# Performance work log

Measured on AMD Instinct MI355X. Metric: run time of the kernel, lower is better.

## Reference

```python
import jax, jax.numpy as jnp
import numpy as np

H = 8
DQ = 32
DK = 32
DV = 32
DC = DQ + DK  # concat dim for additive attention


def setup_inputs() -> dict:
    key = jax.random.key(0)
    ks = jax.random.split(key, 8)
    bs, Lq, Lk = 2, 384, 384
    q = jax.random.normal(ks[0], (bs, Lq, H * DQ), jnp.float32)
    k = jax.random.normal(ks[1], (bs, Lk, H * DK), jnp.float32)
    v = jax.random.normal(ks[2], (bs, Lk, H * DV), jnp.float32)
    q_sequence_lengths = jax.random.randint(ks[3], (bs,), 1, Lq + 1, dtype=jnp.int32)
    k_sequence_lengths = jax.random.randint(ks[4], (bs,), 1, Lk + 1, dtype=jnp.int32)
    bound = 1.0 / np.sqrt(DC)
    w1 = jax.random.uniform(ks[5], (H, DC, DC), jnp.float32, -bound, bound)
    b1 = jax.random.uniform(ks[6], (H, DC), jnp.float32, -bound, bound)
    w2 = jax.random.uniform(ks[7], (H, DC), jnp.float32, -1.0, 1.0)
    return {"q": q, "k": k, "v": v,
            "q_sequence_lengths": q_sequence_lengths,
            "k_sequence_lengths": k_sequence_lengths,
            "w1": w1, "b1": b1, "w2": w2}


def reference(q, k, v, q_sequence_lengths, k_sequence_lengths, w1, b1, w2):
    bs, Lq, _ = q.shape
    Lk = k.shape[1]
    # split heads: (b, h, L, d)
    qh = q.reshape(bs, Lq, H, DQ).transpose(0, 2, 1, 3)
    kh = k.reshape(bs, Lk, H, DK).transpose(0, 2, 1, 3)
    vh = v.reshape(bs, Lk, H, DV).transpose(0, 2, 1, 3)
    # additive scores: tanh(cat(q_i, k_j) @ W1 + b1) @ w2
    # cat @ W1 == q @ W1[:DQ] + k @ W1[DQ:]  (avoids materializing the cat)
    qW = jnp.einsum('bhqd,hde->bhqe', qh, w1[:, :DQ, :])
    kW = jnp.einsum('bhkd,hde->bhke', kh, w1[:, DQ:, :])
    hid = jnp.tanh(qW[:, :, :, None, :] + kW[:, :, None, :, :] + b1[None, :, None, None, :])  # (b,h,q,k,DC)
    scores = jnp.einsum('bhqke,he->bhqk', hid, w2)
    # key-side length mask (end padded)
    kmask = jnp.arange(Lk)[None, :] < k_sequence_lengths[:, None]  # (b, Lk)
    scores = jnp.where(kmask[:, None, None, :], scores, jnp.float32(-1e9))
    att = jax.nn.softmax(scores, axis=-1)  # (b,h,q,k)
    out = jnp.einsum('bhqk,bhkd->bqhd', att, vh)  # (b,q,h,DV)
    # query-side length mask zeros out padded query rows
    qmask = jnp.arange(Lq)[None, :] < q_sequence_lengths[:, None]  # (b, Lq)
    out = out * qmask[:, :, None, None].astype(out.dtype)
    return out.reshape(bs, Lq, H * DV), att
```

## Files before the change

kernel.cpp:

```cpp
#include <hip/hip_runtime.h>

#define NH 8
#define LQ 384
#define LK 384
#define BS 2
#define NQE (BS*NH*LQ*64)

__global__ __launch_bounds__(256) void precompute_kernel(
    const float* __restrict__ qin, const float* __restrict__ kin,
    const float* __restrict__ w1, const float* __restrict__ b1,
    float* __restrict__ ws)
{
    __shared__ float tile[64][65];
    if (blockIdx.x < 1536) {
        int gid = blockIdx.x * 256 + threadIdx.x;
        int e  = gid & 63;
        int qe = gid >> 6;
        int qq = qe % LQ;
        int bh = qe / LQ;
        int b = bh >> 3, h = bh & 7;
        const float* qrow = qin + ((size_t)(b * LQ + qq)) * (NH * 32) + h * 32;
        const float* w1c  = w1 + (size_t)(h * 64) * 64 + e;
        float acc = 0.f;
        #pragma unroll
        for (int d = 0; d < 32; ++d)
            acc = __builtin_fmaf(qrow[d], w1c[d * 64], acc);
        ws[gid] = __expf(acc + acc);
    } else {
        int bid = blockIdx.x - 1536;
        int bh = bid / 6, kt = bid % 6;
        int b = bh >> 3, h = bh & 7;
        int k0 = kt * 64;
        int lane = threadIdx.x & 63, w = threadIdx.x >> 6;
        float w1c[32];
        const float* w1p = w1 + (size_t)(h * 64 + 32) * 64 + lane;
        #pragma unroll
        for (int d = 0; d < 32; ++d) w1c[d] = w1p[d * 64];
        float bv = b1[h * 64 + lane];
        for (int s = 0; s < 16; ++s) {
            int krel = w * 16 + s;
            const float* krow = kin + ((size_t)(b * LK + k0 + krel)) * (NH * 32) + h * 32;
            float acc = bv;
            #pragma unroll
            for (int d = 0; d < 32; ++d)
                acc = __builtin_fmaf(krow[d], w1c[d], acc);
            tile[krel][lane] = __expf(acc + acc);
        }
        __syncthreads();
        float* wk = ws + NQE + (size_t)bh * 64 * LK + k0;
        for (int s = 0; s < 16; ++s) {
            int e = w * 16 + s;
            wk[(size_t)e * LK + lane] = tile[lane][e];
        }
    }
}

__global__ __launch_bounds__(256, 4) void attn_kernel(
    const float* __restrict__ vin,
    const int* __restrict__ qlens, const int* __restrict__ klens,
    const float* __restrict__ w2g, const float* __restrict__ ws,
    float* __restrict__ outg, float* __restrict__ attg)
{
    __shared__ __align__(16) float ek[16 * LK];
    __shared__ __align__(16) float att_s[8][LK];
    __shared__ __align__(16) float eqs[8 * 64];
    __shared__ __align__(16) float w2s[64];

    const int tid = threadIdx.x, wave = tid >> 6, lane = tid & 63;
    const int bh = blockIdx.x / 48, tile = blockIdx.x % 48;
    const int b = bh >> 3, h = bh & 7;
    const int q0 = tile * 8;
    const int klen = klens[b], qlen = qlens[b];

    if (tid < 128) ((float4*)eqs)[tid] = ((const float4*)(ws + ((size_t)bh * LQ + q0) * 64))[tid];
    else if (tid < 144) ((float4*)w2s)[tid - 128] = ((const float4*)(w2g + h * 64))[tid - 128];

    float sc[2][6];
    #pragma unroll
    for (int i = 0; i < 2; ++i)
        #pragma unroll
        for (int j = 0; j < 6; ++j) sc[i][j] = 0.f;

    const float* ekg = ws + NQE + (size_t)bh * 64 * LK;
    for (int ec = 0; ec < 4; ++ec) {
        __syncthreads();
        const float4* src = (const float4*)(ekg + (size_t)ec * 16 * LK);
        #pragma unroll
        for (int r = 0; r < 6; ++r)
            ((float4*)ek)[tid + r * 256] = src[tid + r * 256];
        __syncthreads();
        #pragma unroll 2
        for (int e = 0; e < 16; ++e) {
            float kv[6];
            #pragma unroll
            for (int j = 0; j < 6; ++j) kv[j] = ek[e * LK + j * 64 + lane];
            float wv = w2s[ec * 16 + e];
            #pragma unroll
            for (int i = 0; i < 2; ++i) {
                float qv = eqs[(wave * 2 + i) * 64 + ec * 16 + e];
                #pragma unroll
                for (int j = 0; j < 6; ++j) {
                    float E = qv * kv[j];
                    float r = __builtin_amdgcn_rcpf(1.0f + E);
                    sc[i][j] = __builtin_fmaf(wv, r, sc[i][j]);
                }
            }
        }
    }

    #pragma unroll
    for (int i = 0; i < 2; ++i) {
        int row = wave * 2 + i, q = q0 + row;
        float s_[6], p[6];
        float m = -3.4e38f;
        #pragma unroll
        for (int j = 0; j < 6; ++j) {
            int kk = j * 64 + lane;
            float v = -2.0f * sc[i][j];
            s_[j] = (kk < klen) ? v : -3.4e38f;
            m = fmaxf(m, s_[j]);
        }
        #pragma unroll
        for (int off = 32; off >= 1; off >>= 1) m = fmaxf(m, __shfl_xor(m, off));
        float ssum = 0.f;
        #pragma unroll
        for (int j = 0; j < 6; ++j) {
            int kk = j * 64 + lane;
            p[j] = (kk < klen) ? __expf(s_[j] - m) : 0.f;
            ssum += p[j];
        }
        #pragma unroll
        for (int off = 32; off >= 1; off >>= 1) ssum += __shfl_xor(ssum, off);
        float inv = __builtin_amdgcn_rcpf(ssum);
        float* arow = att_s[row];
        float* ag = attg + ((size_t)(bh * LQ + q)) * LK;
        #pragma unroll
        for (int j = 0; j < 6; ++j) {
            float a = p[j] * inv;
            arow[j * 64 + lane] = a;
            ag[j * 64 + lane]   = a;
        }
    }

    const int dv = lane & 31, halfk = lane >> 5;
    float oacc[2] = {0.f, 0.f};
    for (int c = 0; c < 2; ++c) {
        __syncthreads();
        const float4* vg = (const float4*)(vin + ((size_t)(b * LK + c * 192)) * (NH * 32) + h * 32);
        #pragma unroll
        for (int r = 0; r < 6; ++r) {
            int fidx = tid + r * 256;
            int kk = fidx >> 3, d4 = fidx & 7;
            ((float4*)ek)[fidx] = vg[(size_t)kk * 64 + d4];
        }
        __syncthreads();
        #pragma unroll
        for (int i = 0; i < 2; ++i) {
            const float* ar = att_s[wave * 2 + i] + c * 192 + halfk * 96;
            const float* vb = ek + (halfk * 96) * 32 + dv;
            float acc = 0.f;
            #pragma unroll
            for (int kk = 0; kk < 96; kk += 4) {
                float4 a4 = *(const float4*)(ar + kk);
                acc = __builtin_fmaf(a4.x, vb[(kk + 0) * 32], acc);
                acc = __builtin_fmaf(a4.y, vb[(kk + 1) * 32], acc);
                acc = __builtin_fmaf(a4.z, vb[(kk + 2) * 32], acc);
                acc = __builtin_fmaf(a4.w, vb[(kk + 3) * 32], acc);
            }
            oacc[i] += acc;
        }
    }
    #pragma unroll
    for (int i = 0; i < 2; ++i) oacc[i] += __shfl_xor(oacc[i], 32);
    if (lane < 32) {
        #pragma unroll
        for (int i = 0; i < 2; ++i) {
            int q = q0 + wave * 2 + i;
            outg[((size_t)(b * LQ + q)) * (NH * 32) + h * 32 + dv] = (q < qlen) ? oacc[i] : 0.f;
        }
    }
}

extern "C" void kernel_launch(void* const* d_in, const int* in_sizes, int n_in,
                              void* d_out, int out_size, void* d_ws, size_t ws_size,
                              hipStream_t stream) {
    const float* q    = (const float*)d_in[0];
    const float* k    = (const float*)d_in[1];
    const float* v    = (const float*)d_in[2];
    const int*   qlen = (const int*)d_in[3];
    const int*   klen = (const int*)d_in[4];
    const float* w1   = (const float*)d_in[5];
    const float* b1   = (const float*)d_in[6];
    const float* w2   = (const float*)d_in[7];
    float* out = (float*)d_out;
    float* att = out + (size_t)BS * LQ * NH * 32;
    float* ws  = (float*)d_ws;

    precompute_kernel<<<1632, 256, 0, stream>>>(q, k, w1, b1, ws);
    attn_kernel<<<768, 256, 0, stream>>>(v, qlen, klen, w2, ws, out, att);
}
```

Baseline: 113.5 us.

## Merge four reciprocals per score step, fuse q projection into attention kernel

The score loop now combines four terms w_i/(1+E_i) into one fraction, so it needs a single reciprocal per four hidden units instead of one each, cutting transcendental-unit pressure. The q-side exp projection moves out of the precompute kernel and into the attention kernel, which removes a workspace round trip and shrinks the precompute grid to the k side only. The P·V loop is re-laid out so each lane reads float4 of V and writes float4 outputs, with a shuffle reduction across k groups. The risk is overflow or precision loss in the product of four (1+E) terms when the exponentials get large.

```diff
diff --git a/kernel.cpp b/kernel.cpp
--- a/kernel.cpp
+++ b/kernel.cpp
@@ -4,61 +4,48 @@
 #define LQ 384
 #define LK 384
 #define BS 2
-#define NQE (BS*NH*LQ*64)
-
-__global__ __launch_bounds__(256) void precompute_kernel(
-    const float* __restrict__ qin, const float* __restrict__ kin,
-    const float* __restrict__ w1, const float* __restrict__ b1,
-    float* __restrict__ ws)
+
+__global__ __launch_bounds__(256) void pre_ek_kernel(
+    const float* __restrict__ kin, const float* __restrict__ w1,
+    const float* __restrict__ b1, float* __restrict__ ws)
 {
-    __shared__ float tile[64][65];
-    if (blockIdx.x < 1536) {
-        int gid = blockIdx.x * 256 + threadIdx.x;
-        int e  = gid & 63;
-        int qe = gid >> 6;
-        int qq = qe % LQ;
-        int bh = qe / LQ;
-        int b = bh >> 3, h = bh & 7;
-        const float* qrow = qin + ((size_t)(b * LQ + qq)) * (NH * 32) + h * 32;
-        const float* w1c  = w1 + (size_t)(h * 64) * 64 + e;
-        float acc = 0.f;
-        #pragma unroll
-        for (int d = 0; d < 32; ++d)
-            acc = __builtin_fmaf(qrow[d], w1c[d * 64], acc);
-        ws[gid] = __expf(acc + acc);
-    } else {
-        int bid = blockIdx.x - 1536;
-        int bh = bid / 6, kt = bid % 6;
-        int b = bh >> 3, h = bh & 7;
-        int k0 = kt * 64;
-        int lane = threadIdx.x & 63, w = threadIdx.x >> 6;
-        float w1c[32];
-        const float* w1p = w1 + (size_t)(h * 64 + 32) * 64 + lane;
-        #pragma unroll
-        for (int d = 0; d < 32; ++d) w1c[d] = w1p[d * 64];
-        float bv = b1[h * 64 + lane];
-        for (int s = 0; s < 16; ++s) {
-            int krel = w * 16 + s;
-            const float* krow = kin + ((size_t)(b * LK + k0 + krel)) * (NH * 32) + h * 32;
-            float acc = bv;
-            #pragma unroll
-            for (int d = 0; d < 32; ++d)
-                acc = __builtin_fmaf(krow[d], w1c[d], acc);
-            tile[krel][lane] = __expf(acc + acc);
-        }
-        __syncthreads();
-        float* wk = ws + NQE + (size_t)bh * 64 * LK + k0;
-        for (int s = 0; s < 16; ++s) {
-            int e = w * 16 + s;
-            wk[(size_t)e * LK + lane] = tile[lane][e];
-        }
+    __shared__ float tile[32][65];
+    const int bid = blockIdx.x;
+    const int bh = bid / 12, kt = bid % 12;
+    const int b = bh >> 3, h = bh & 7;
+    const int k0 = kt * 32;
+    const int lane = threadIdx.x & 63, w = threadIdx.x >> 6;
+
+    float w1c[32];
+    const float* w1p = w1 + (size_t)(h * 64 + 32) * 64 + lane;
+    #pragma unroll
+    for (int d = 0; d < 32; ++d) w1c[d] = w1p[d * 64];
+    const float bv = b1[h * 64 + lane];
+
+    #pragma unroll
+    for (int s = 0; s < 8; ++s) {
+        int kr = w * 8 + s;
+        const float* krow = kin + ((size_t)(b * LK + k0 + kr)) * (NH * 32) + h * 32;
+        float acc = bv;
+        #pragma unroll
+        for (int d = 0; d < 32; ++d) acc = __builtin_fmaf(krow[d], w1c[d], acc);
+        tile[kr][lane] = __expf(acc + acc);
+    }
+    __syncthreads();
+    float* wk = ws + (size_t)bh * 64 * LK + k0;
+    const int k32 = lane & 31, eh = lane >> 5;
+    #pragma unroll
+    for (int s2 = 0; s2 < 8; ++s2) {
+        int e = w * 16 + s2 * 2 + eh;
+        wk[(size_t)e * LK + k32] = tile[k32][e];
     }
 }
 
 __global__ __launch_bounds__(256, 4) void attn_kernel(
-    const float* __restrict__ vin,
+    const float* __restrict__ qin, const float* __restrict__ vin,
     const int* __restrict__ qlens, const int* __restrict__ klens,
-    const float* __restrict__ w2g, const float* __restrict__ ws,
+    const float* __restrict__ w1, const float* __restrict__ w2g,
+    const float* __restrict__ ws,
     float* __restrict__ outg, float* __restrict__ attg)
 {
     __shared__ __align__(16) float ek[16 * LK];
@@ -72,8 +59,24 @@
     const int q0 = tile * 8;
     const int klen = klens[b], qlen = qlens[b];
 
-    if (tid < 128) ((float4*)eqs)[tid] = ((const float4*)(ws + ((size_t)bh * LQ + q0) * 64))[tid];
-    else if (tid < 144) ((float4*)w2s)[tid - 128] = ((const float4*)(w2g + h * 64))[tid - 128];
+    if (tid < 16) ((float4*)w2s)[tid] = ((const float4*)(w2g + h * 64))[tid];
+
+    {
+        float w1c[32];
+        const float* w1q = w1 + (size_t)(h * 64) * 64 + lane;
+        #pragma unroll
+        for (int d = 0; d < 32; ++d) w1c[d] = w1q[d * 64];
+        const float* qr0 = qin + ((size_t)(b * LQ + q0 + wave)) * (NH * 32) + h * 32;
+        const float* qr1 = qr0 + 4 * (NH * 32);
+        float a0 = 0.f, a1 = 0.f;
+        #pragma unroll
+        for (int d = 0; d < 32; ++d) {
+            a0 = __builtin_fmaf(qr0[d], w1c[d], a0);
+            a1 = __builtin_fmaf(qr1[d], w1c[d], a1);
+        }
+        eqs[wave * 64 + lane]       = __expf(a0 + a0);
+        eqs[(wave + 4) * 64 + lane] = __expf(a1 + a1);
+    }
 
     float sc[2][6];
     #pragma unroll
@@ -81,7 +84,10 @@
         #pragma unroll
         for (int j = 0; j < 6; ++j) sc[i][j] = 0.f;
 
-    const float* ekg = ws + NQE + (size_t)bh * 64 * LK;
+    const float* ekg = ws + (size_t)bh * 64 * LK;
+    const float4* eq0p = (const float4*)(eqs + (wave * 2 + 0) * 64);
+    const float4* eq1p = (const float4*)(eqs + (wave * 2 + 1) * 64);
+
     for (int ec = 0; ec < 4; ++ec) {
         __syncthreads();
         const float4* src = (const float4*)(ekg + (size_t)ec * 16 * LK);
@@ -89,20 +95,39 @@
         for (int r = 0; r < 6; ++r)
             ((float4*)ek)[tid + r * 256] = src[tid + r * 256];
         __syncthreads();
-        #pragma unroll 2
-        for (int e = 0; e < 16; ++e) {
-            float kv[6];
+        #pragma unroll
+        for (int q4 = 0; q4 < 4; ++q4) {
+            float4 wv  = ((const float4*)w2s)[ec * 4 + q4];
+            float4 eqv0 = eq0p[ec * 4 + q4];
+            float4 eqv1 = eq1p[ec * 4 + q4];
+            const float* ekb = ek + (q4 * 4) * LK + lane;
             #pragma unroll
-            for (int j = 0; j < 6; ++j) kv[j] = ek[e * LK + j * 64 + lane];
-            float wv = w2s[ec * 16 + e];
-            #pragma unroll
-            for (int i = 0; i < 2; ++i) {
-                float qv = eqs[(wave * 2 + i) * 64 + ec * 16 + e];
-                #pragma unroll
-                for (int j = 0; j < 6; ++j) {
-                    float E = qv * kv[j];
-                    float r = __builtin_amdgcn_rcpf(1.0f + E);
-                    sc[i][j] = __builtin_fmaf(wv, r, sc[i][j]);
+            for (int j = 0; j < 6; ++j) {
+                float kv0 = ekb[j * 64];
+                float kv1 = ekb[LK + j * 64];
+                float kv2 = ekb[2 * LK + j * 64];
+                float kv3 = ekb[3 * LK + j * 64];
+                {
+                    float t0 = __builtin_fmaf(eqv0.x, kv0, 1.f);
+                    float t1 = __builtin_fmaf(eqv0.y, kv1, 1.f);
+                    float t2 = __builtin_fmaf(eqv0.z, kv2, 1.f);
+                    float t3 = __builtin_fmaf(eqv0.w, kv3, 1.f);
+                    float p12 = t0 * t1, p34 = t2 * t3;
+                    float n12 = wv.x * t1; n12 = __builtin_fmaf(wv.y, t0, n12);
+                    float n34 = wv.z * t3; n34 = __builtin_fmaf(wv.w, t2, n34);
+                    float num = n12 * p34; num = __builtin_fmaf(n34, p12, num);
+                    sc[0][j] = __builtin_fmaf(num, __builtin_amdgcn_rcpf(p12 * p34), sc[0][j]);
+                }
+                {
+                    float t0 = __builtin_fmaf(eqv1.x, kv0, 1.f);
+                    float t1 = __builtin_fmaf(eqv1.y, kv1, 1.f);
+                    float t2 = __builtin_fmaf(eqv1.z, kv2, 1.f);
+                    float t3 = __builtin_fmaf(eqv1.w, kv3, 1.f);
+                    float p12 = t0 * t1, p34 = t2 * t3;
+                    float n12 = wv.x * t1; n12 = __builtin_fmaf(wv.y, t0, n12);
+                    float n34 = wv.z * t3; n34 = __builtin_fmaf(wv.w, t2, n34);
+                    float num = n12 * p34; num = __builtin_fmaf(n34, p12, num);
+                    sc[1][j] = __builtin_fmaf(num, __builtin_amdgcn_rcpf(p12 * p34), sc[1][j]);
                 }
             }
         }
@@ -142,8 +167,10 @@
         }
     }
 
-    const int dv = lane & 31, halfk = lane >> 5;
-    float oacc[2] = {0.f, 0.f};
+    const int kf = lane >> 3, dg = lane & 7;
+    float oa[2][4] = {{0.f,0.f,0.f,0.f},{0.f,0.f,0.f,0.f}};
+    const float* ar0 = att_s[wave * 2 + 0];
+    const float* ar1 = att_s[wave * 2 + 1];
     for (int c = 0; c < 2; ++c) {
         __syncthreads();
         const float4* vg = (const float4*)(vin + ((size_t)(b * LK + c * 192)) * (NH * 32) + h * 32);
@@ -154,29 +181,43 @@
             ((float4*)ek)[fidx] = vg[(size_t)kk * 64 + d4];
         }
         __syncthreads();
-        #pragma unroll
-        for (int i = 0; i < 2; ++i) {
-            const float* ar = att_s[wave * 2 + i] + c * 192 + halfk * 96;
-            const float* vb = ek + (halfk * 96) * 32 + dv;
-            float acc = 0.f;
-            #pragma unroll
-            for (int kk = 0; kk < 96; kk += 4) {
-                float4 a4 = *(const float4*)(ar + kk);
-                acc = __builtin_fmaf(a4.x, vb[(kk + 0) * 32], acc);
-                acc = __builtin_fmaf(a4.y, vb[(kk + 1) * 32], acc);
-                acc = __builtin_fmaf(a4.z, vb[(kk + 2) * 32], acc);
-                acc = __builtin_fmaf(a4.w, vb[(kk + 3) * 32], acc);
-            }
-            oacc[i] += acc;
-        }
-    }
-    #pragma unroll
-    for (int i = 0; i < 2; ++i) oacc[i] += __shfl_xor(oacc[i], 32);
-    if (lane < 32) {
+        const float* a0p = ar0 + c * 192;
+        const float* a1p = ar1 + c * 192;
+        #pragma unroll 6
+        for (int k0 = 0; k0 < 192; k0 += 8) {
+            float4 vv = ((const float4*)ek)[(k0 + kf) * 8 + dg];
+            float a0 = a0p[k0 + kf];
+            float a1 = a1p[k0 + kf];
+            oa[0][0] = __builtin_fmaf(a0, vv.x, oa[0][0]);
+            oa[0][1] = __builtin_fmaf(a0, vv.y, oa[0][1]);
+            oa[0][2] = __builtin_fmaf(a0, vv.z, oa[0][2]);
+            oa[0][3] = __builtin_fmaf(a0, vv.w, oa[0][3]);
+            oa[1][0] = __builtin_fmaf(a1, vv.x, oa[1][0]);
+            oa[1][1] = __builtin_fmaf(a1, vv.y, oa[1][1]);
+            oa[1][2] = __builtin_fmaf(a1, vv.z, oa[1][2]);
+            oa[1][3] = __builtin_fmaf(a1, vv.w, oa[1][3]);
+        }
+    }
+    #pragma unroll
+    for (int i = 0; i < 2; ++i)
+        #pragma unroll
+        for (int u = 0; u < 4; ++u) {
+            float x = oa[i][u];
+            x += __shfl_xor(x, 8);
+            x += __shfl_xor(x, 16);
+            x += __shfl_xor(x, 32);
+            oa[i][u] = x;
+        }
+    if (kf == 0) {
         #pragma unroll
         for (int i = 0; i < 2; ++i) {
             int q = q0 + wave * 2 + i;
-            outg[((size_t)(b * LQ + q)) * (NH * 32) + h * 32 + dv] = (q < qlen) ? oacc[i] : 0.f;
+            float4 o4;
+            o4.x = (q < qlen) ? oa[i][0] : 0.f;
+            o4.y = (q < qlen) ? oa[i][1] : 0.f;
+            o4.z = (q < qlen) ? oa[i][2] : 0.f;
+            o4.w = (q < qlen) ? oa[i][3] : 0.f;
+            ((float4*)(outg + ((size_t)(b * LQ + q)) * (NH * 32) + h * 32))[dg] = o4;
         }
     }
 }
@@ -196,6 +237,6 @@
     float* att = out + (size_t)BS * LQ * NH * 32;
     float* ws  = (float*)d_ws;
 
-    precompute_kernel<<<1632, 256, 0, stream>>>(q, k, w1, b1, ws);
-    attn_kernel<<<768, 256, 0, stream>>>(v, qlen, klen, w2, ws, out, att);
+    pre_ek_kernel<<<192, 256, 0, stream>>>(k, w1, b1, ws);
+    attn_kernel<<<768, 256, 0, stream>>>(q, v, qlen, klen, w1, w2, ws, out, att);
 }
```

Result: slower. 157.2 us (+38.6%).
